# Kernel optimization log

Measured on AMD Instinct MI355X. Metric: run time of the kernel, lower is better.

The kernel has to match this reference:

```python
import jax, jax.numpy as jnp
import numpy as np


def _maxpool2(x):
    # 2x2 max pool, stride 2, on NCHW
    b, c, h, w = x.shape
    return x.reshape(b, c, h // 2, 2, w // 2, 2).max(axis=(3, 5))


def _conv1x1(w, x):
    # w: [out_c, in_c], x: [B, in_c, H, W]
    return jnp.einsum('oc,bchw->bohw', w, x)


def setup_inputs() -> dict:
    key = jax.random.key(0)
    ks = jax.random.split(key, 5)
    B, C, H, W = 16, 64, 64, 64
    x = jax.random.normal(ks[0], (B, C, H, W), dtype=jnp.float32)
    # 1x1 conv weights (spectral-norm treated as already-normalized params)
    Wt = jax.random.normal(ks[1], (C // 8, C), dtype=jnp.float32) * 0.05
    Wp = jax.random.normal(ks[2], (C // 8, C), dtype=jnp.float32) * 0.05
    Wg = jax.random.normal(ks[3], (C // 2, C), dtype=jnp.float32) * 0.05
    Wo = jax.random.normal(ks[4], (C, C // 2), dtype=jnp.float32) * 0.05
    gamma = jnp.float32(0.5)  # nonzero so attention branch contributes
    return {"x": x, "Wt": Wt, "Wp": Wp, "Wg": Wg, "Wo": Wo, "gamma": gamma}


def reference(x, Wt, Wp, Wg, Wo, gamma):
    b, c, h, w = x.shape
    theta = _conv1x1(Wt, x).reshape(b, c // 8, h * w)            # [B, C/8, HW]
    phi = _maxpool2(_conv1x1(Wp, x)).reshape(b, c // 8, -1)      # [B, C/8, HW/4]
    g = _maxpool2(_conv1x1(Wg, x)).reshape(b, c // 2, -1)        # [B, C/2, HW/4]
    # scores: [B, HW, HW/4]; softmax over pooled (key) axis
    beta = jax.nn.softmax(jnp.einsum('bct,bcs->bts', theta, phi), axis=-1)
    o = jnp.einsum('bcs,bts->bct', g, beta).reshape(b, c // 2, h, w)
    o = _conv1x1(Wo, o)                                          # [B, C, H, W]
    return gamma * o + x
```

## Files before the change

kernel.cpp:

```cpp
#include <hip/hip_runtime.h>
#include <math.h>

#define NB   16
#define NC   64
#define HWs  4096
#define NPS  1024
#define LOG2E 1.44269504088896341f

static constexpr size_t PHI_OFF = (size_t)NB * HWs * 8;
static constexpr size_t GT_OFF  = PHI_OFF + (size_t)NB * NPS * 8;

typedef short s16x8 __attribute__((ext_vector_type(8)));
typedef float f32x4 __attribute__((ext_vector_type(4)));

#define LD8G(p) (*(const s16x8*)(p))

__device__ inline unsigned short f2bf(float f) {
    unsigned int u = __float_as_uint(f);
    u += 0x7fffu + ((u >> 16) & 1u);
    return (unsigned short)(u >> 16);
}
__device__ inline unsigned int pk2(float a, float b) {
    unsigned int ua = __float_as_uint(a); ua += 0x7fffu + ((ua >> 16) & 1u);
    unsigned int ub = __float_as_uint(b); ub += 0x7fffu + ((ub >> 16) & 1u);
    return (ua >> 16) | (ub & 0xffff0000u);
}

__global__ __launch_bounds__(256) void k_proj(
    const float* __restrict__ x, const float* __restrict__ Wt,
    const float* __restrict__ Wp, const float* __restrict__ Wg,
    unsigned short* __restrict__ ws)
{
    __shared__ float xs[64 * 128];

    unsigned short* theta = ws;
    unsigned short* phi   = ws + PHI_OFF;
    unsigned short* gT    = ws + GT_OFF;

    const int tid = threadIdx.x;
    const int blk = blockIdx.x;
    const int b   = blk >> 5;
    const int rp  = blk & 31;

    const float* xsrc = x + (size_t)b * NC * HWs + rp * 128;
#pragma unroll
    for (int i = 0; i < 8; ++i) {
        const int idx = i * 256 + tid;
        const int ci  = idx >> 5;
        const int f4  = idx & 31;
        float4 v = *(const float4*)(xsrc + (size_t)ci * HWs + f4 * 4);
        *(float4*)(xs + ci * 128 + f4 * 4) = v;
    }
    __syncthreads();

    const int h    = tid & 127;
    const int half = __builtin_amdgcn_readfirstlane(tid >> 7);
    const int row  = h & 1;
    const int col  = h >> 1;
    const int px   = row * 64 + col;

    float a8[8], ag[16];
#pragma unroll
    for (int j = 0; j < 8; ++j)  a8[j] = 0.f;
#pragma unroll
    for (int j = 0; j < 16; ++j) ag[j] = 0.f;

    const float* W8 = half ? Wp : Wt;
    const float* WG = Wg + half * 16 * NC;

#pragma unroll 4
    for (int ci = 0; ci < NC; ++ci) {
        const float xv = xs[ci * 128 + px];
#pragma unroll
        for (int j = 0; j < 8; ++j)  a8[j] += W8[j * NC + ci] * xv;
#pragma unroll
        for (int j = 0; j < 16; ++j) ag[j] += WG[j * NC + ci] * xv;
    }

    if (half == 0) {
        const int q = (2 * rp + row) * 64 + col;
        uint4 pkd;
        pkd.x = pk2(a8[0] * LOG2E, a8[1] * LOG2E);
        pkd.y = pk2(a8[2] * LOG2E, a8[3] * LOG2E);
        pkd.z = pk2(a8[4] * LOG2E, a8[5] * LOG2E);
        pkd.w = pk2(a8[6] * LOG2E, a8[7] * LOG2E);
        *(uint4*)(theta + ((size_t)b * HWs + q) * 8) = pkd;
    }

#pragma unroll
    for (int j = 0; j < 8; ++j) {
        float v = a8[j];
        v = fmaxf(v, __shfl_xor(v, 1));
        v = fmaxf(v, __shfl_xor(v, 2));
        a8[j] = v;
    }
#pragma unroll
    for (int j = 0; j < 16; ++j) {
        float v = ag[j];
        v = fmaxf(v, __shfl_xor(v, 1));
        v = fmaxf(v, __shfl_xor(v, 2));
        ag[j] = v;
    }

    if ((h & 3) == 0) {
        const int ps = rp * 32 + (h >> 2);
        if (half == 1) {
            uint4 pkd;
            pkd.x = pk2(a8[0], a8[1]); pkd.y = pk2(a8[2], a8[3]);
            pkd.z = pk2(a8[4], a8[5]); pkd.w = pk2(a8[6], a8[7]);
            *(uint4*)(phi + ((size_t)b * NPS + ps) * 8) = pkd;
        }
#pragma unroll
        for (int j = 0; j < 16; ++j) {
            const int c = half * 16 + j;
            gT[((size_t)b * 32 + c) * NPS + ps] = f2bf(ag[j]);
        }
    }
}

__global__ __launch_bounds__(256, 4) void k_attn(
    const float* __restrict__ x, const float* __restrict__ Wo,
    const float* __restrict__ gamma_p, const unsigned short* __restrict__ ws,
    float* __restrict__ out)
{
    __shared__ __align__(16) unsigned char smem[18432];

    const int tid  = threadIdx.x;
    const int wave = __builtin_amdgcn_readfirstlane(tid >> 6);
    const int lane = tid & 63;
    const int quad = lane >> 4, lr = lane & 15;
    const int blk  = blockIdx.x;
    const int b    = blk >> 6;
    const int q0   = (blk & 63) * 64;

    const unsigned short* th = ws + (size_t)b * HWs * 8;
    const unsigned short* ph = ws + PHI_OFF + (size_t)b * NPS * 8;
    const unsigned short* gp = ws + GT_OFF + (size_t)b * 32 * NPS;
    unsigned short* Pw = (unsigned short*)smem + wave * 2304;

    const s16x8 zf = {0, 0, 0, 0, 0, 0, 0, 0};
    const f32x4 zc = {0.f, 0.f, 0.f, 0.f};

    const s16x8 thA = (quad == 0) ? LD8G(th + (size_t)(q0 + wave * 16 + lr) * 8) : zf;

    f32x4 O[2];
    f32x4 l4;
#pragma unroll
    for (int r = 0; r < 4; ++r) { O[0][r] = 0.f; O[1][r] = 0.f; l4[r] = 0.f; }

    s16x8 phB_e[4], phB_o[4];
    s16x8 Gf_e[2][2], Gf_o[2][2];

#define LOADPH(dst, tile)                                                     \
    _Pragma("unroll")                                                         \
    for (int ss = 0; ss < 4; ++ss)                                            \
        dst[ss] = LD8G(ph + (size_t)((tile) * 64 + ss * 16 + lr) * 8);

#define LOADG(dst, tile)                                                      \
    _Pragma("unroll")                                                         \
    for (int kc = 0; kc < 2; ++kc)                                            \
        _Pragma("unroll")                                                     \
        for (int cs = 0; cs < 2; ++cs)                                        \
            dst[kc][cs] = LD8G(gp + (size_t)(cs * 16 + lr) * NPS +            \
                               (tile) * 64 + kc * 32 + quad * 8);

#define QK(Sv, phB)                                                           \
    _Pragma("unroll")                                                         \
    for (int ss = 0; ss < 4; ++ss)                                            \
        Sv[ss] = __builtin_amdgcn_mfma_f32_16x16x32_bf16(thA, phB[ss], zc, 0, 0, 0);

#define EXPST(Sv, wbuf)                                                       \
    _Pragma("unroll")                                                         \
    for (int ss = 0; ss < 4; ++ss)                                            \
        _Pragma("unroll")                                                     \
        for (int r = 0; r < 4; ++r) {                                         \
            const float p = exp2f(Sv[ss][r]);                                 \
            l4[r] += p;                                                       \
            Pw[(wbuf) + (quad * 4 + r) * 72 + ss * 16 + lr] =                 \
                (unsigned short)(__float_as_uint(p) >> 16);                   \
        }

#define BODY(phCUR, GfPREV, GfCUR, phNXT, curT, rbuf, wbuf)                   \
    {                                                                         \
        LOADG(GfCUR, (curT));                                                 \
        LOADPH(phNXT, (curT) + 1);                                            \
        const s16x8 Pf0 = *(const s16x8*)(Pw + (rbuf) + lr * 72 + quad * 8);  \
        const s16x8 Pf1 = *(const s16x8*)(Pw + (rbuf) + lr * 72 + 32 + quad * 8); \
        f32x4 S[4];                                                           \
        QK(S, phCUR);                                                         \
        _Pragma("unroll")                                                     \
        for (int cs = 0; cs < 2; ++cs)                                        \
            O[cs] = __builtin_amdgcn_mfma_f32_16x16x32_bf16(Pf0, GfPREV[0][cs], O[cs], 0, 0, 0); \
        _Pragma("unroll")                                                     \
        for (int cs = 0; cs < 2; ++cs)                                        \
            O[cs] = __builtin_amdgcn_mfma_f32_16x16x32_bf16(Pf1, GfPREV[1][cs], O[cs], 0, 0, 0); \
        EXPST(S, wbuf);                                                       \
    }

    LOADPH(phB_e, 0);
    {
        LOADG(Gf_e, 0);
        LOADPH(phB_o, 1);
        f32x4 S[4];
        QK(S, phB_e);
        EXPST(S, 0);
    }

    for (int t = 1; t < 15; t += 2) {
        BODY(phB_o, Gf_e, Gf_o, phB_e, t,     0,    1152);
        BODY(phB_e, Gf_o, Gf_e, phB_o, t + 1, 1152, 0);
    }

    {
        LOADG(Gf_o, 15);
        const s16x8 Pf0 = *(const s16x8*)(Pw + 0 + lr * 72 + quad * 8);
        const s16x8 Pf1 = *(const s16x8*)(Pw + 0 + lr * 72 + 32 + quad * 8);
        f32x4 S[4];
        QK(S, phB_o);
#pragma unroll
        for (int cs = 0; cs < 2; ++cs)
            O[cs] = __builtin_amdgcn_mfma_f32_16x16x32_bf16(Pf0, Gf_e[0][cs], O[cs], 0, 0, 0);
#pragma unroll
        for (int cs = 0; cs < 2; ++cs)
            O[cs] = __builtin_amdgcn_mfma_f32_16x16x32_bf16(Pf1, Gf_e[1][cs], O[cs], 0, 0, 0);
        EXPST(S, 1152);
    }

    {
        const s16x8 Pf0 = *(const s16x8*)(Pw + 1152 + lr * 72 + quad * 8);
        const s16x8 Pf1 = *(const s16x8*)(Pw + 1152 + lr * 72 + 32 + quad * 8);
#pragma unroll
        for (int cs = 0; cs < 2; ++cs)
            O[cs] = __builtin_amdgcn_mfma_f32_16x16x32_bf16(Pf0, Gf_o[0][cs], O[cs], 0, 0, 0);
#pragma unroll
        for (int cs = 0; cs < 2; ++cs)
            O[cs] = __builtin_amdgcn_mfma_f32_16x16x32_bf16(Pf1, Gf_o[1][cs], O[cs], 0, 0, 0);
    }

#pragma unroll
    for (int r = 0; r < 4; ++r) {
        float v = l4[r];
        v += __shfl_xor(v, 1);
        v += __shfl_xor(v, 2);
        v += __shfl_xor(v, 4);
        v += __shfl_xor(v, 8);
        l4[r] = 1.f / v;
    }

    __syncthreads();
    float* otile = (float*)smem;
#pragma unroll
    for (int cs = 0; cs < 2; ++cs) {
        f32x4 v;
#pragma unroll
        for (int r = 0; r < 4; ++r) v[r] = O[cs][r] * l4[r];
        *(f32x4*)(otile + (cs * 16 + lr) * 68 + wave * 16 + quad * 4) = v;
    }
    __syncthreads();

    const int qq = tid & 63;
    const int quarter = __builtin_amdgcn_readfirstlane(tid >> 6);
    float acc[16];
#pragma unroll
    for (int j = 0; j < 16; ++j) acc[j] = 0.f;
    for (int c = 0; c < 32; ++c) {
        const float ov = otile[c * 68 + qq];
#pragma unroll
        for (int j = 0; j < 16; ++j)
            acc[j] += Wo[(quarter * 16 + j) * 32 + c] * ov;
    }
    const float gam = gamma_p[0];
#pragma unroll
    for (int j = 0; j < 16; ++j) {
        const size_t a = ((size_t)b * NC + quarter * 16 + j) * HWs + q0 + qq;
        out[a] = gam * acc[j] + x[a];
    }
}

extern "C" void kernel_launch(void* const* d_in, const int* in_sizes, int n_in,
                              void* d_out, int out_size, void* d_ws, size_t ws_size,
                              hipStream_t stream) {
    const float* x     = (const float*)d_in[0];
    const float* Wt    = (const float*)d_in[1];
    const float* Wp    = (const float*)d_in[2];
    const float* Wg    = (const float*)d_in[3];
    const float* Wo    = (const float*)d_in[4];
    const float* gamma = (const float*)d_in[5];
    float* out = (float*)d_out;
    unsigned short* ws = (unsigned short*)d_ws;

    k_proj<<<512, 256, 0, stream>>>(x, Wt, Wp, Wg, ws);
    k_attn<<<1024, 256, 0, stream>>>(x, Wo, gamma, ws, out);
}
```

Before: 133.0 us.

## Split projection work across twice the blocks and add scheduling barriers in attention

The projection kernel now runs 1024 blocks instead of 512, and each block handles half of the output channels, so each thread keeps fewer accumulators. The cost is that each block reloads the same x tile, doubling x reads. In the attention loop, sched_barrier calls are placed around the QK/PV MFMA section to stop the compiler from interleaving the exp/store code with the matrix ops. That pins the instruction order, but it may also block useful overlap of latency.

```diff
diff --git a/kernel.cpp b/kernel.cpp
--- a/kernel.cpp
+++ b/kernel.cpp
@@ -14,6 +14,7 @@
 typedef float f32x4 __attribute__((ext_vector_type(4)));
 
 #define LD8G(p) (*(const s16x8*)(p))
+#define SB()    __builtin_amdgcn_sched_barrier(0)
 
 __device__ inline unsigned short f2bf(float f) {
     unsigned int u = __float_as_uint(f);
@@ -37,10 +38,11 @@
     unsigned short* phi   = ws + PHI_OFF;
     unsigned short* gT    = ws + GT_OFF;
 
-    const int tid = threadIdx.x;
-    const int blk = blockIdx.x;
-    const int b   = blk >> 5;
-    const int rp  = blk & 31;
+    const int tid  = threadIdx.x;
+    const int blk  = blockIdx.x;
+    const int b    = blk >> 6;
+    const int rp   = (blk >> 1) & 31;
+    const int half = blk & 1;
 
     const float* xsrc = x + (size_t)b * NC * HWs + rp * 128;
 #pragma unroll
@@ -53,67 +55,66 @@
     }
     __syncthreads();
 
-    const int h    = tid & 127;
-    const int half = __builtin_amdgcn_readfirstlane(tid >> 7);
-    const int row  = h & 1;
-    const int col  = h >> 1;
-    const int px   = row * 64 + col;
-
-    float a8[8], ag[16];
-#pragma unroll
-    for (int j = 0; j < 8; ++j)  a8[j] = 0.f;
-#pragma unroll
-    for (int j = 0; j < 16; ++j) ag[j] = 0.f;
-
-    const float* W8 = half ? Wp : Wt;
-    const float* WG = Wg + half * 16 * NC;
+    const int h   = tid & 127;
+    const int sub = __builtin_amdgcn_readfirstlane(tid >> 7);
+    const int row = h & 1;
+    const int col = h >> 1;
+    const int px  = row * 64 + col;
+
+    float a4[4], ag8[8];
+#pragma unroll
+    for (int j = 0; j < 4; ++j) a4[j] = 0.f;
+#pragma unroll
+    for (int j = 0; j < 8; ++j) ag8[j] = 0.f;
+
+    const float* W8 = (half ? Wp : Wt) + sub * 4 * NC;
+    const float* WG = Wg + (half * 16 + sub * 8) * NC;
 
 #pragma unroll 4
     for (int ci = 0; ci < NC; ++ci) {
         const float xv = xs[ci * 128 + px];
 #pragma unroll
-        for (int j = 0; j < 8; ++j)  a8[j] += W8[j * NC + ci] * xv;
-#pragma unroll
-        for (int j = 0; j < 16; ++j) ag[j] += WG[j * NC + ci] * xv;
+        for (int j = 0; j < 4; ++j) a4[j] += W8[j * NC + ci] * xv;
+#pragma unroll
+        for (int j = 0; j < 8; ++j) ag8[j] += WG[j * NC + ci] * xv;
     }
 
     if (half == 0) {
         const int q = (2 * rp + row) * 64 + col;
-        uint4 pkd;
-        pkd.x = pk2(a8[0] * LOG2E, a8[1] * LOG2E);
-        pkd.y = pk2(a8[2] * LOG2E, a8[3] * LOG2E);
-        pkd.z = pk2(a8[4] * LOG2E, a8[5] * LOG2E);
-        pkd.w = pk2(a8[6] * LOG2E, a8[7] * LOG2E);
-        *(uint4*)(theta + ((size_t)b * HWs + q) * 8) = pkd;
+        uint2 pkd;
+        pkd.x = pk2(a4[0] * LOG2E, a4[1] * LOG2E);
+        pkd.y = pk2(a4[2] * LOG2E, a4[3] * LOG2E);
+        *(uint2*)(theta + ((size_t)b * HWs + q) * 8 + sub * 4) = pkd;
+    } else {
+#pragma unroll
+        for (int j = 0; j < 4; ++j) {
+            float v = a4[j];
+            v = fmaxf(v, __shfl_xor(v, 1));
+            v = fmaxf(v, __shfl_xor(v, 2));
+            a4[j] = v;
+        }
     }
 
 #pragma unroll
     for (int j = 0; j < 8; ++j) {
-        float v = a8[j];
+        float v = ag8[j];
         v = fmaxf(v, __shfl_xor(v, 1));
         v = fmaxf(v, __shfl_xor(v, 2));
-        a8[j] = v;
-    }
-#pragma unroll
-    for (int j = 0; j < 16; ++j) {
-        float v = ag[j];
-        v = fmaxf(v, __shfl_xor(v, 1));
-        v = fmaxf(v, __shfl_xor(v, 2));
-        ag[j] = v;
+        ag8[j] = v;
     }
 
     if ((h & 3) == 0) {
         const int ps = rp * 32 + (h >> 2);
         if (half == 1) {
-            uint4 pkd;
-            pkd.x = pk2(a8[0], a8[1]); pkd.y = pk2(a8[2], a8[3]);
-            pkd.z = pk2(a8[4], a8[5]); pkd.w = pk2(a8[6], a8[7]);
-            *(uint4*)(phi + ((size_t)b * NPS + ps) * 8) = pkd;
+            uint2 pkd;
+            pkd.x = pk2(a4[0], a4[1]);
+            pkd.y = pk2(a4[2], a4[3]);
+            *(uint2*)(phi + ((size_t)b * NPS + ps) * 8 + sub * 4) = pkd;
         }
 #pragma unroll
-        for (int j = 0; j < 16; ++j) {
-            const int c = half * 16 + j;
-            gT[((size_t)b * 32 + c) * NPS + ps] = f2bf(ag[j]);
+        for (int j = 0; j < 8; ++j) {
+            const int c = half * 16 + sub * 8 + j;
+            gT[((size_t)b * 32 + c) * NPS + ps] = f2bf(ag8[j]);
         }
     }
 }
@@ -186,6 +187,7 @@
         LOADPH(phNXT, (curT) + 1);                                            \
         const s16x8 Pf0 = *(const s16x8*)(Pw + (rbuf) + lr * 72 + quad * 8);  \
         const s16x8 Pf1 = *(const s16x8*)(Pw + (rbuf) + lr * 72 + 32 + quad * 8); \
+        SB();                                                                 \
         f32x4 S[4];                                                           \
         QK(S, phCUR);                                                         \
         _Pragma("unroll")                                                     \
@@ -194,6 +196,7 @@
         _Pragma("unroll")                                                     \
         for (int cs = 0; cs < 2; ++cs)                                        \
             O[cs] = __builtin_amdgcn_mfma_f32_16x16x32_bf16(Pf1, GfPREV[1][cs], O[cs], 0, 0, 0); \
+        SB();                                                                 \
         EXPST(S, wbuf);                                                       \
     }
 
@@ -201,8 +204,10 @@
     {
         LOADG(Gf_e, 0);
         LOADPH(phB_o, 1);
+        SB();
         f32x4 S[4];
         QK(S, phB_e);
+        SB();
         EXPST(S, 0);
     }
 
@@ -215,6 +220,7 @@
         LOADG(Gf_o, 15);
         const s16x8 Pf0 = *(const s16x8*)(Pw + 0 + lr * 72 + quad * 8);
         const s16x8 Pf1 = *(const s16x8*)(Pw + 0 + lr * 72 + 32 + quad * 8);
+        SB();
         f32x4 S[4];
         QK(S, phB_o);
 #pragma unroll
@@ -223,6 +229,7 @@
 #pragma unroll
         for (int cs = 0; cs < 2; ++cs)
             O[cs] = __builtin_amdgcn_mfma_f32_16x16x32_bf16(Pf1, Gf_e[1][cs], O[cs], 0, 0, 0);
+        SB();
         EXPST(S, 1152);
     }
 
@@ -289,6 +296,6 @@
     float* out = (float*)d_out;
     unsigned short* ws = (unsigned short*)d_ws;
 
-    k_proj<<<512, 256, 0, stream>>>(x, Wt, Wp, Wg, ws);
+    k_proj<<<1024, 256, 0, stream>>>(x, Wt, Wp, Wg, ws);
     k_attn<<<1024, 256, 0, stream>>>(x, Wo, gamma, ws, out);
 }
```

Result: faster. 127.2 us (-4.4%).
